# Performance work log

Measured on AMD Instinct MI355X. Metric: run time of the kernel, lower is better.

The kernel has to match this reference:

```python
import jax, jax.numpy as jnp
import numpy as np

B, H, D, V = 1024, 4, 256, 100000


def setup_inputs() -> dict:
    key = jax.random.key(0)
    k1, k2, k3, k4 = jax.random.split(key, 4)
    x = jax.random.normal(k1, (B, D), dtype=jnp.float32)
    # Glorot-normal-ish scaling for the learned matrices
    proj_mat = jax.random.normal(k2, (H * D, D), dtype=jnp.float32) * (2.0 / (H * D + D)) ** 0.5
    mix_mat = jax.random.normal(k3, (H, D), dtype=jnp.float32) * (2.0 / (H + D)) ** 0.5
    emb = jax.random.normal(k4, (V, D), dtype=jnp.float32) * 0.05
    return {"x": x, "proj_mat": proj_mat, "mix_mat": mix_mat, "emb": emb}


def reference(x, proj_mat, mix_mat, emb):
    # per-head projection: [B, H*D] -> [B, H, D]
    proj = jnp.tanh(x @ proj_mat.T).reshape(B, H, D)
    # mixture weights over heads: [B, H]
    pi = jax.nn.softmax(x @ mix_mat.T, axis=-1)
    # full-vocab logits per head: [B, H, V]
    head_logits = jnp.einsum("bhd,vd->bhv", proj, emb)
    head_probs = jax.nn.softmax(head_logits, axis=-1)
    # weighted mixture over heads -> [B, V]
    probs = jnp.einsum("bh,bhv->bv", pi, head_probs)
    return probs
```

## Files before the change

### kernel.cpp

```cpp
#include <hip/hip_runtime.h>
#include <stdint.h>


#define VOCAB 100000
#define NVB 391
#define VPAD 100096

typedef __attribute__((ext_vector_type(8))) short short8;
typedef __attribute__((ext_vector_type(4))) float f32x4;

__device__ __forceinline__ short f2bf(float f) {
  uint32_t u = __float_as_uint(f);
  u = (u + 0x7FFFu + ((u >> 16) & 1u)) >> 16;
  return (short)u;
}

#define VMCNT0() asm volatile("s_waitcnt vmcnt(0)" ::: "memory")
#define LGKM0()  asm volatile("s_waitcnt lgkmcnt(0)" ::: "memory")
#define SCHED0() __builtin_amdgcn_sched_barrier(0)
#define BAR()    __builtin_amdgcn_s_barrier()

__global__ __launch_bounds__(256) void proj_kernel(const float* __restrict__ x,
                                                   const float* __restrict__ pm,
                                                   short* __restrict__ projA) {
  __shared__ float xs[64][36];
  __shared__ float ps[64][36];
  const int tid = threadIdx.x;
  const int tx = tid & 15, ty = tid >> 4;
  const int m0 = blockIdx.y * 64, n0 = blockIdx.x * 64;
  float acc[4][4];
#pragma unroll
  for (int i = 0; i < 4; i++)
#pragma unroll
    for (int j = 0; j < 4; j++) acc[i][j] = 0.f;

  for (int k0 = 0; k0 < 256; k0 += 32) {
    const int r = tid >> 2, c = (tid & 3) * 8;
    *(float4*)&xs[r][c]     = *(const float4*)&x[(m0 + r) * 256 + k0 + c];
    *(float4*)&xs[r][c + 4] = *(const float4*)&x[(m0 + r) * 256 + k0 + c + 4];
    *(float4*)&ps[r][c]     = *(const float4*)&pm[(n0 + r) * 256 + k0 + c];
    *(float4*)&ps[r][c + 4] = *(const float4*)&pm[(n0 + r) * 256 + k0 + c + 4];
    __syncthreads();
#pragma unroll
    for (int kk = 0; kk < 32; kk += 4) {
      float4 xa[4], pb[4];
#pragma unroll
      for (int i = 0; i < 4; i++) xa[i] = *(const float4*)&xs[ty * 4 + i][kk];
#pragma unroll
      for (int j = 0; j < 4; j++) pb[j] = *(const float4*)&ps[tx * 4 + j][kk];
#pragma unroll
      for (int i = 0; i < 4; i++)
#pragma unroll
        for (int j = 0; j < 4; j++)
          acc[i][j] += xa[i].x * pb[j].x + xa[i].y * pb[j].y +
                       xa[i].z * pb[j].z + xa[i].w * pb[j].w;
    }
    __syncthreads();
  }
#pragma unroll
  for (int i = 0; i < 4; i++)
#pragma unroll
    for (int j = 0; j < 4; j++)
      projA[(size_t)(m0 + ty * 4 + i) * 1024 + (n0 + tx * 4 + j)] = f2bf(tanhf(acc[i][j]));
}

__global__ __launch_bounds__(256) void pi_kernel(const float* __restrict__ x,
                                                 const float* __restrict__ mm,
                                                 float* __restrict__ pi) {
  int b = blockIdx.x * 256 + threadIdx.x;
  if (b >= 1024) return;
  float acc[4] = {0.f, 0.f, 0.f, 0.f};
  for (int k = 0; k < 256; k += 4) {
    float4 xv = *(const float4*)&x[(size_t)b * 256 + k];
#pragma unroll
    for (int h = 0; h < 4; h++) {
      float4 mv = *(const float4*)&mm[h * 256 + k];
      acc[h] += xv.x * mv.x + xv.y * mv.y + xv.z * mv.z + xv.w * mv.w;
    }
  }
  float mx = fmaxf(fmaxf(acc[0], acc[1]), fmaxf(acc[2], acc[3]));
  float e[4], ssum = 0.f;
#pragma unroll
  for (int h = 0; h < 4; h++) { e[h] = __expf(acc[h] - mx); ssum += e[h]; }
#pragma unroll
  for (int h = 0; h < 4; h++) pi[b * 4 + h] = e[h] / ssum;
}

__global__ __launch_bounds__(256) void embB_kernel(const float* __restrict__ emb,
                                                   short* __restrict__ embB) {
  size_t i = ((size_t)blockIdx.x * 256 + threadIdx.x) * 8;
  size_t row = i >> 8;
  short8 b8;
  if (row < VOCAB) {
    float4 f0 = *(const float4*)&emb[i];
    float4 f1 = *(const float4*)&emb[i + 4];
    b8[0] = f2bf(f0.x); b8[1] = f2bf(f0.y); b8[2] = f2bf(f0.z); b8[3] = f2bf(f0.w);
    b8[4] = f2bf(f1.x); b8[5] = f2bf(f1.y); b8[6] = f2bf(f1.z); b8[7] = f2bf(f1.w);
  } else {
#pragma unroll
    for (int j = 0; j < 8; ++j) b8[j] = 0;
  }
  *(short8*)&embB[i] = b8;
}


template <int KT>
__device__ __forceinline__ void stage_A(const char* gA, char* sm, int wid) {
  constexpr int NXT = (KT + 1) & 1;
#pragma unroll
  for (int h = 0; h < 2; ++h)
#pragma unroll
    for (int j = 0; j < 2; ++j)
      __builtin_amdgcn_global_load_lds(
          (const __attribute__((address_space(1))) void*)(gA + (KT + 1) * 128 + h * 65536 + j * 32768),
          (__attribute__((address_space(3))) void*)(sm + NXT * 65536 + h * 16384 + j * 8192 + wid * 1024),
          16, 0, 0);
}
template <int KT>
__device__ __forceinline__ void stage_B(const char* gB, char* sm, int wid) {
  constexpr int NXT = (KT + 1) & 1;
#pragma unroll
  for (int h = 0; h < 2; ++h)
#pragma unroll
    for (int j = 0; j < 2; ++j)
      __builtin_amdgcn_global_load_lds(
          (const __attribute__((address_space(1))) void*)(gB + (KT + 1) * 128 + h * 65536 + j * 32768),
          (__attribute__((address_space(3))) void*)(sm + NXT * 65536 + 32768 + h * 16384 + j * 8192 + wid * 1024),
          16, 0, 0);
}

#define MFMA_CLUSTER(AHALF, BSEL, MOFF, NOFF)                                              \
  __builtin_amdgcn_s_setprio(1);                                                           \
  _Pragma("unroll") for (int ks = 0; ks < 2; ++ks)                                         \
      _Pragma("unroll") for (int i = 0; i < 4; ++i)                                        \
          _Pragma("unroll") for (int j = 0; j < 2; ++j)                                    \
              acc[(MOFF) + i][(NOFF) + j] = __builtin_amdgcn_mfma_f32_16x16x32_bf16(       \
                  AHALF[i][ks], BSEL[j][ks], acc[(MOFF) + i][(NOFF) + j], 0, 0, 0);        \
  __builtin_amdgcn_s_setprio(0);

template <int KT>
__device__ __forceinline__ void k_step(char* sm, const char* gA, const char* gB, int wid,
                                       f32x4 (&acc)[8][4], int aK0, int aK1, int bK0, int bK1) {
  constexpr int CB = (KT & 1) * 65536;
  short8 a[4][2], b0[2][2], b1[2][2];
#pragma unroll
  for (int i = 0; i < 4; ++i) {
    a[i][0] = *(const short8*)(sm + CB + aK0 + i * 2048);
    a[i][1] = *(const short8*)(sm + CB + aK1 + i * 2048);
  }
#pragma unroll
  for (int j = 0; j < 2; ++j) {
    b0[j][0] = *(const short8*)(sm + CB + bK0 + j * 2048);
    b0[j][1] = *(const short8*)(sm + CB + bK1 + j * 2048);
  }
  if (KT < 3) stage_A<KT>(gA, sm, wid);
  BAR();
  LGKM0();
  SCHED0();
  MFMA_CLUSTER(a, b0, 0, 0);
  BAR();
#pragma unroll
  for (int j = 0; j < 2; ++j) {
    b1[j][0] = *(const short8*)(sm + CB + bK0 + (2 + j) * 2048);
    b1[j][1] = *(const short8*)(sm + CB + bK1 + (2 + j) * 2048);
  }
  if (KT < 3) stage_B<KT>(gB, sm, wid);
  BAR();
  LGKM0();
  SCHED0();
  MFMA_CLUSTER(a, b1, 0, 2);
  BAR();
#pragma unroll
  for (int i = 0; i < 4; ++i) {
    a[i][0] = *(const short8*)(sm + CB + aK0 + (4 + i) * 2048);
    a[i][1] = *(const short8*)(sm + CB + aK1 + (4 + i) * 2048);
  }
  BAR();
  LGKM0();
  SCHED0();
  MFMA_CLUSTER(a, b1, 4, 2);
  VMCNT0();
  BAR();
  MFMA_CLUSTER(a, b0, 4, 0);
}

template <int MODE>
__global__ __launch_bounds__(512, 2) void mos_gemm8(const short* __restrict__ projA_s,
                                                    const short* __restrict__ embB_s,
                                                    const float* __restrict__ w,
                                                    float* __restrict__ part,
                                                    float* __restrict__ out) {
  __shared__ __align__(16) char sm[131072];
  const int tid = threadIdx.x;
  const int lane = tid & 63, wid = tid >> 6;
  const int wr = wid >> 2, wc = wid & 3;
  const int l15 = lane & 15, l4 = lane >> 4;
  const int m0 = blockIdx.x * 256;
  const int v0 = blockIdx.y * 256;

  const int cxor = ((tid & 7) ^ ((tid >> 3) & 7)) * 16;
  const char* gA = (const char*)projA_s + (size_t)(m0 + (tid >> 3)) * 512 + cxor;
  const char* gB = (const char*)embB_s + (size_t)(v0 + (tid >> 3)) * 512 + cxor;

  const int sA = l15 & 7;
  const int aK0 = (wr * 128 + l15) * 128 + ((l4 ^ sA) << 4);
  const int aK1 = (wr * 128 + l15) * 128 + (((4 + l4) ^ sA) << 4);
  const int bK0 = 32768 + (wc * 64 + l15) * 128 + ((l4 ^ sA) << 4);
  const int bK1 = 32768 + (wc * 64 + l15) * 128 + (((4 + l4) ^ sA) << 4);

  f32x4 acc[8][4];
#pragma unroll
  for (int i = 0; i < 8; ++i)
#pragma unroll
    for (int j = 0; j < 4; ++j) acc[i][j] = (f32x4){0.f, 0.f, 0.f, 0.f};

  stage_A<-1>(gA, sm, wid);
  stage_B<-1>(gB, sm, wid);
  SCHED0();
  VMCNT0();
  BAR();

  k_step<0>(sm, gA, gB, wid, acc, aK0, aK1, bK0, bK1);
  k_step<1>(sm, gA, gB, wid, acc, aK0, aK1, bK0, bK1);
  k_step<2>(sm, gA, gB, wid, acc, aK0, aK1, bK0, bK1);
  k_step<3>(sm, gA, gB, wid, acc, aK0, aK1, bK0, bK1);

  if (MODE == 0) {
#pragma unroll
    for (int mi = 0; mi < 8; ++mi) {
      float p[4] = {0.f, 0.f, 0.f, 0.f};
#pragma unroll
      for (int ni = 0; ni < 4; ++ni) {
        int v = v0 + wc * 64 + ni * 16 + l15;
        bool ok = v < VOCAB;
#pragma unroll
        for (int r = 0; r < 4; ++r) {
          float e = __expf(acc[mi][ni][r]);
          p[r] += ok ? e : 0.f;
        }
      }
#pragma unroll
      for (int r = 0; r < 4; ++r) {
        p[r] += __shfl_xor(p[r], 1, 64);
        p[r] += __shfl_xor(p[r], 2, 64);
        p[r] += __shfl_xor(p[r], 4, 64);
        p[r] += __shfl_xor(p[r], 8, 64);
      }
      if (l15 == 0) {
        float4 pv = {p[0], p[1], p[2], p[3]};
        *(float4*)(sm + (wc * 256 + wr * 128 + mi * 16 + l4 * 4) * 4) = pv;
      }
    }
    __syncthreads();
    if (tid < 256) {
      const float* rf = (const float*)sm;
      float ssum = rf[tid] + rf[256 + tid] + rf[512 + tid] + rf[768 + tid];
      part[(size_t)blockIdx.y * 4096 + m0 + tid] = ssum;
    }
  } else {
#pragma unroll
    for (int mi = 0; mi < 8; ++mi) {
      int mbase = m0 + wr * 128 + mi * 16;
      float4 wv = *(const float4*)&w[mbase + l4 * 4];
      size_t brow = (size_t)(mbase >> 2) + l4;
#pragma unroll
      for (int ni = 0; ni < 4; ++ni) {
        int v = v0 + wc * 64 + ni * 16 + l15;
        float val = wv.x * __expf(acc[mi][ni][0]) + wv.y * __expf(acc[mi][ni][1]) +
                    wv.z * __expf(acc[mi][ni][2]) + wv.w * __expf(acc[mi][ni][3]);
        if (v < VOCAB) out[brow * VOCAB + v] = val;
      }
    }
  }
}

__global__ __launch_bounds__(256) void reduce_w(const float* __restrict__ part,
                                                const float* __restrict__ pi,
                                                float* __restrict__ w) {
  int m = blockIdx.x * 256 + threadIdx.x;
  float sum = 0.f;
  for (int c = 0; c < NVB; ++c) sum += part[(size_t)c * 4096 + m];
  w[m] = pi[m] / sum;
}

extern "C" void kernel_launch(void* const* d_in, const int* in_sizes, int n_in,
                              void* d_out, int out_size, void* d_ws, size_t ws_size,
                              hipStream_t stream) {
  const float* x        = (const float*)d_in[0];
  const float* proj_mat = (const float*)d_in[1];
  const float* mix_mat  = (const float*)d_in[2];
  const float* emb      = (const float*)d_in[3];
  float* out = (float*)d_out;

  char* ws = (char*)d_ws;
  short* projA = (short*)ws;
  float* pi    = (float*)(ws + (2u << 20));
  float* w     = (float*)(ws + (2u << 20) + 16384);
  short* embB  = (short*)(ws + (4u << 20));
  float* part  = (float*)(ws + (4u << 20) + (size_t)VPAD * 512);

  dim3 g1(16, 16);
  proj_kernel<<<g1, 256, 0, stream>>>(x, proj_mat, projA);
  pi_kernel<<<4, 256, 0, stream>>>(x, mix_mat, pi);
  embB_kernel<<<VPAD * 32 / 256, 256, 0, stream>>>(emb, embB);

  dim3 gg(16, NVB);
  mos_gemm8<0><<<gg, 512, 0, stream>>>(projA, embB, nullptr, part, nullptr);
  reduce_w<<<16, 256, 0, stream>>>(part, pi, w);
  mos_gemm8<1><<<gg, 512, 0, stream>>>(projA, embB, w, nullptr, out);
}
```

Measured before the change: 684.2 us.

## Restructure GEMM k-loop pipeline and swizzle block order for XCD locality

Each k-step now issues the combined A/B global-to-LDS prefetch for the next tile at its start and waits with a partial vmcnt, so only the previous batch of loads must land. It then computes with two large MFMA clusters and fewer barriers, replacing four interleaved load/compute phases. The grid becomes 1D with a swizzle that gives each XCD a contiguous range of vocab tiles, aiming to improve L2 reuse of the embedding tiles. The risks are higher register pressure, since all B fragments and both A halves are held live, and less interleaving of LDS reads with MFMA work.

```diff
diff --git a/kernel.cpp b/kernel.cpp
--- a/kernel.cpp
+++ b/kernel.cpp
@@ -15,7 +15,7 @@
   return (short)u;
 }
 
-#define VMCNT0() asm volatile("s_waitcnt vmcnt(0)" ::: "memory")
+#define VMCNT(n) asm volatile("s_waitcnt vmcnt(" #n ")" ::: "memory")
 #define LGKM0()  asm volatile("s_waitcnt lgkmcnt(0)" ::: "memory")
 #define SCHED0() __builtin_amdgcn_sched_barrier(0)
 #define BAR()    __builtin_amdgcn_s_barrier()
@@ -104,84 +104,77 @@
 }
 
 
-template <int KT>
-__device__ __forceinline__ void stage_A(const char* gA, char* sm, int wid) {
-  constexpr int NXT = (KT + 1) & 1;
+__device__ __forceinline__ void stage_AB(const char* gA, const char* gB, char* sm,
+                                         int buf, int kt, int wid) {
 #pragma unroll
   for (int h = 0; h < 2; ++h)
 #pragma unroll
-    for (int j = 0; j < 2; ++j)
+    for (int j = 0; j < 2; ++j) {
       __builtin_amdgcn_global_load_lds(
-          (const __attribute__((address_space(1))) void*)(gA + (KT + 1) * 128 + h * 65536 + j * 32768),
-          (__attribute__((address_space(3))) void*)(sm + NXT * 65536 + h * 16384 + j * 8192 + wid * 1024),
+          (const __attribute__((address_space(1))) void*)(gA + kt * 128 + h * 65536 + j * 32768),
+          (__attribute__((address_space(3))) void*)(sm + buf * 65536 + h * 16384 + j * 8192 + wid * 1024),
           16, 0, 0);
-}
-template <int KT>
-__device__ __forceinline__ void stage_B(const char* gB, char* sm, int wid) {
-  constexpr int NXT = (KT + 1) & 1;
-#pragma unroll
-  for (int h = 0; h < 2; ++h)
-#pragma unroll
-    for (int j = 0; j < 2; ++j)
       __builtin_amdgcn_global_load_lds(
-          (const __attribute__((address_space(1))) void*)(gB + (KT + 1) * 128 + h * 65536 + j * 32768),
-          (__attribute__((address_space(3))) void*)(sm + NXT * 65536 + 32768 + h * 16384 + j * 8192 + wid * 1024),
+          (const __attribute__((address_space(1))) void*)(gB + kt * 128 + h * 65536 + j * 32768),
+          (__attribute__((address_space(3))) void*)(sm + buf * 65536 + 32768 + h * 16384 + j * 8192 + wid * 1024),
           16, 0, 0);
-}
-
-#define MFMA_CLUSTER(AHALF, BSEL, MOFF, NOFF)                                              \
-  __builtin_amdgcn_s_setprio(1);                                                           \
-  _Pragma("unroll") for (int ks = 0; ks < 2; ++ks)                                         \
-      _Pragma("unroll") for (int i = 0; i < 4; ++i)                                        \
-          _Pragma("unroll") for (int j = 0; j < 2; ++j)                                    \
-              acc[(MOFF) + i][(NOFF) + j] = __builtin_amdgcn_mfma_f32_16x16x32_bf16(       \
-                  AHALF[i][ks], BSEL[j][ks], acc[(MOFF) + i][(NOFF) + j], 0, 0, 0);        \
-  __builtin_amdgcn_s_setprio(0);
+    }
+}
 
 template <int KT>
 __device__ __forceinline__ void k_step(char* sm, const char* gA, const char* gB, int wid,
                                        f32x4 (&acc)[8][4], int aK0, int aK1, int bK0, int bK1) {
   constexpr int CB = (KT & 1) * 65536;
-  short8 a[4][2], b0[2][2], b1[2][2];
+  if (KT < 3) {
+    stage_AB(gA, gB, sm, (KT + 1) & 1, KT + 1, wid);
+    SCHED0();
+    VMCNT(8);
+  } else {
+    SCHED0();
+    VMCNT(0);
+  }
+  BAR();
+  SCHED0();
+
+  short8 b[4][2], a0[4][2], a1[4][2];
+#pragma unroll
+  for (int j = 0; j < 4; ++j) {
+    b[j][0] = *(const short8*)(sm + CB + bK0 + j * 2048);
+    b[j][1] = *(const short8*)(sm + CB + bK1 + j * 2048);
+  }
 #pragma unroll
   for (int i = 0; i < 4; ++i) {
-    a[i][0] = *(const short8*)(sm + CB + aK0 + i * 2048);
-    a[i][1] = *(const short8*)(sm + CB + aK1 + i * 2048);
-  }
-#pragma unroll
-  for (int j = 0; j < 2; ++j) {
-    b0[j][0] = *(const short8*)(sm + CB + bK0 + j * 2048);
-    b0[j][1] = *(const short8*)(sm + CB + bK1 + j * 2048);
-  }
-  if (KT < 3) stage_A<KT>(gA, sm, wid);
-  BAR();
+    a0[i][0] = *(const short8*)(sm + CB + aK0 + i * 2048);
+    a0[i][1] = *(const short8*)(sm + CB + aK1 + i * 2048);
+  }
+  __builtin_amdgcn_s_setprio(1);
+#pragma unroll
+  for (int ks = 0; ks < 2; ++ks)
+#pragma unroll
+    for (int i = 0; i < 4; ++i)
+#pragma unroll
+      for (int j = 0; j < 4; ++j)
+        acc[i][j] = __builtin_amdgcn_mfma_f32_16x16x32_bf16(a0[i][ks], b[j][ks], acc[i][j], 0, 0, 0);
+  __builtin_amdgcn_s_setprio(0);
+#pragma unroll
+  for (int i = 0; i < 4; ++i) {
+    a1[i][0] = *(const short8*)(sm + CB + aK0 + (4 + i) * 2048);
+    a1[i][1] = *(const short8*)(sm + CB + aK1 + (4 + i) * 2048);
+  }
   LGKM0();
   SCHED0();
-  MFMA_CLUSTER(a, b0, 0, 0);
   BAR();
-#pragma unroll
-  for (int j = 0; j < 2; ++j) {
-    b1[j][0] = *(const short8*)(sm + CB + bK0 + (2 + j) * 2048);
-    b1[j][1] = *(const short8*)(sm + CB + bK1 + (2 + j) * 2048);
-  }
-  if (KT < 3) stage_B<KT>(gB, sm, wid);
-  BAR();
-  LGKM0();
   SCHED0();
-  MFMA_CLUSTER(a, b1, 0, 2);
-  BAR();
-#pragma unroll
-  for (int i = 0; i < 4; ++i) {
-    a[i][0] = *(const short8*)(sm + CB + aK0 + (4 + i) * 2048);
-    a[i][1] = *(const short8*)(sm + CB + aK1 + (4 + i) * 2048);
-  }
-  BAR();
-  LGKM0();
-  SCHED0();
-  MFMA_CLUSTER(a, b1, 4, 2);
-  VMCNT0();
-  BAR();
-  MFMA_CLUSTER(a, b0, 4, 0);
+  __builtin_amdgcn_s_setprio(1);
+#pragma unroll
+  for (int ks = 0; ks < 2; ++ks)
+#pragma unroll
+    for (int i = 0; i < 4; ++i)
+#pragma unroll
+      for (int j = 0; j < 4; ++j)
+        acc[4 + i][j] =
+            __builtin_amdgcn_mfma_f32_16x16x32_bf16(a1[i][ks], b[j][ks], acc[4 + i][j], 0, 0, 0);
+  __builtin_amdgcn_s_setprio(0);
 }
 
 template <int MODE>
@@ -195,8 +188,12 @@
   const int lane = tid & 63, wid = tid >> 6;
   const int wr = wid >> 2, wc = wid & 3;
   const int l15 = lane & 15, l4 = lane >> 4;
-  const int m0 = blockIdx.x * 256;
-  const int v0 = blockIdx.y * 256;
+
+  const int id = blockIdx.x;
+  const int sw = (id & 7) * 782 + (id >> 3);
+  const int vb = sw >> 4, mb = sw & 15;
+  const int m0 = mb * 256;
+  const int v0 = vb * 256;
 
   const int cxor = ((tid & 7) ^ ((tid >> 3) & 7)) * 16;
   const char* gA = (const char*)projA_s + (size_t)(m0 + (tid >> 3)) * 512 + cxor;
@@ -214,11 +211,8 @@
 #pragma unroll
     for (int j = 0; j < 4; ++j) acc[i][j] = (f32x4){0.f, 0.f, 0.f, 0.f};
 
-  stage_A<-1>(gA, sm, wid);
-  stage_B<-1>(gB, sm, wid);
+  stage_AB(gA, gB, sm, 0, 0, wid);
   SCHED0();
-  VMCNT0();
-  BAR();
 
   k_step<0>(sm, gA, gB, wid, acc, aK0, aK1, bK0, bK1);
   k_step<1>(sm, gA, gB, wid, acc, aK0, aK1, bK0, bK1);
@@ -255,7 +249,7 @@
     if (tid < 256) {
       const float* rf = (const float*)sm;
       float ssum = rf[tid] + rf[256 + tid] + rf[512 + tid] + rf[768 + tid];
-      part[(size_t)blockIdx.y * 4096 + m0 + tid] = ssum;
+      part[(size_t)vb * 4096 + m0 + tid] = ssum;
     }
   } else {
 #pragma unroll
@@ -302,10 +296,9 @@
   dim3 g1(16, 16);
   proj_kernel<<<g1, 256, 0, stream>>>(x, proj_mat, projA);
   pi_kernel<<<4, 256, 0, stream>>>(x, mix_mat, pi);
-  embB_kernel<<<VPAD * 32 / 256, 256, 0, stream>>>(emb, embB);
-
-  dim3 gg(16, NVB);
-  mos_gemm8<0><<<gg, 512, 0, stream>>>(projA, embB, nullptr, part, nullptr);
+  embB_kernel<<<VPAD / 8, 256, 0, stream>>>(emb, embB);
+
+  mos_gemm8<0><<<16 * NVB, 512, 0, stream>>>(projA, embB, nullptr, part, nullptr);
   reduce_w<<<16, 256, 0, stream>>>(part, pi, w);
-  mos_gemm8<1><<<gg, 512, 0, stream>>>(projA, embB, w, nullptr, out);
-}
+  mos_gemm8<1><<<16 * NVB, 512, 0, stream>>>(projA, embB, w, nullptr, out);
+}
```

Result: no change. 688.0 us (+0.6%).
